# Kernel tuning notes

Hardware: AMD Instinct MI355X
Metric: run time of the kernel (lower is better)

The kernel has to match this reference:

```python
import jax, jax.numpy as jnp
import numpy as np

B, L, H, HEADS = 32, 512, 1024, 16
LN_EPS = 1e-5
NEG_INF = -1e9


def _layernorm(x, g, b):
    m = jnp.mean(x, axis=-1, keepdims=True)
    v = jnp.mean(jnp.square(x - m), axis=-1, keepdims=True)
    return (x - m) * jax.lax.rsqrt(v + LN_EPS) * g + b


def setup_inputs() -> dict:
    key = jax.random.key(0)
    ks = jax.random.split(key, 10)
    # deterministic variable graph sizes -> padding mask with fixed total valid count
    lengths = L - (np.arange(B) % 16) * 8          # per-graph node counts
    mask_np = np.arange(L)[None, :] < lengths[:, None]   # [B, L] bool
    node_idx = np.nonzero(mask_np.reshape(-1))[0].astype(np.int32)  # [14464]
    s = 0.02
    inp = {
        "x_dense": jax.random.normal(ks[0], (B, L, H), jnp.float32),
        "batch_CLS": jax.random.normal(ks[1], (B, 1, H), jnp.float32),
        "mask": jnp.asarray(mask_np),
        "node_idx": jnp.asarray(node_idx),
        "WQ": jax.random.normal(ks[2], (H, H), jnp.float32) * s,
        "bQ": jnp.zeros((H,), jnp.float32),
        "WK": jax.random.normal(ks[3], (H, H), jnp.float32) * s,
        "bK": jnp.zeros((H,), jnp.float32),
        "WV": jax.random.normal(ks[4], (H, H), jnp.float32) * s,
        "bV": jnp.zeros((H,), jnp.float32),
        "WO": jax.random.normal(ks[5], (H, H), jnp.float32) * s,
        "bO": jnp.zeros((H,), jnp.float32),
        "g1": jnp.ones((H,), jnp.float32),
        "beta1": jnp.zeros((H,), jnp.float32),
        "Wf1": jax.random.normal(ks[6], (H, 2 * H), jnp.float32) * s,
        "bf1": jnp.zeros((2 * H,), jnp.float32),
        "Wf2": jax.random.normal(ks[7], (2 * H, H), jnp.float32) * s,
        "bf2": jnp.zeros((H,), jnp.float32),
        "g2": jnp.ones((H,), jnp.float32),
        "beta2": jnp.zeros((H,), jnp.float32),
    }
    return inp


def reference(x_dense, batch_CLS, mask, node_idx, WQ, bQ, WK, bK, WV, bV,
              WO, bO, g1, beta1, Wf1, bf1, Wf2, bf2, g2, beta2):
    b, l, h = x_dense.shape
    d = h // HEADS
    # append CLS token; attention mask gets an always-True CLS column
    xd = jnp.concatenate([x_dense, batch_CLS], axis=1)            # [B, S, H], S = L+1
    am = jnp.concatenate([mask, jnp.ones((b, 1), bool)], axis=1)  # [B, S]
    S = l + 1
    Qh = (xd @ WQ + bQ).reshape(b, S, HEADS, d)
    Kh = (xd @ WK + bK).reshape(b, S, HEADS, d)
    Vh = (xd @ WV + bV).reshape(b, S, HEADS, d)
    scores = jnp.einsum('bqhd,bkhd->bhqk', Qh, Kh) / jnp.sqrt(jnp.float32(d))
    # additive padding mask over keys (masked_attention=True, clustering=False)
    scores = scores + jnp.where(am, 0.0, NEG_INF)[:, None, None, :]
    A = jax.nn.softmax(scores, axis=-1)                           # [B, h, S, S]
    # torch layout: A_torch[hh*B + b] == A[b, hh] -> cls_attn [h*B, S]
    cls_attn = jax.lax.stop_gradient(
        jnp.transpose(A[:, :, -1, :], (1, 0, 2)).reshape(HEADS * b, S))
    ctx = jnp.einsum('bhqk,bkhd->bqhd', A, Vh).reshape(b, S, h)
    attn_out = ctx @ WO + bO + xd                                  # residual
    cls_rows = attn_out[:, -1, :]                                  # [B, H]
    nodes = attn_out[:, :-1, :].reshape(b * l, h)[node_idx]        # valid nodes packed
    packed = jnp.concatenate([nodes, cls_rows], axis=0)            # [Ntot+B, H]
    h1 = _layernorm(packed, g1, beta1)
    ffn = jax.nn.relu(h1 @ Wf1 + bf1) @ Wf2 + bf2
    out = _layernorm(ffn + h1, g2, beta2)
    return out, cls_attn
```

## Files before the change

### kernel.cpp

```cpp
#include <hip/hip_runtime.h>
#include <stdint.h>

typedef unsigned short ushort_t;
typedef __bf16 bf16x8 __attribute__((ext_vector_type(8)));
typedef float  f32x4  __attribute__((ext_vector_type(4)));
typedef unsigned short ushortx8 __attribute__((ext_vector_type(8)));

constexpr int CB  = 32;
constexpr int CL  = 512;
constexpr int CNH = 16;
constexpr int CDH = 64;
constexpr int CS  = 513;
constexpr int CNR = CB * CS;
constexpr int CVTS = 576;
constexpr int CST = 136;

__device__ __forceinline__ float bf2f(ushort_t u) {
  return __builtin_bit_cast(float, (uint32_t)u << 16);
}
__device__ __forceinline__ ushort_t f2bf(float f) {
  __bf16 h = (__bf16)f;
  return __builtin_bit_cast(ushort_t, h);
}

typedef __attribute__((address_space(1))) const unsigned int GU32;
typedef __attribute__((address_space(3))) unsigned int LU32;
__device__ __forceinline__ void gld16(const void* g, void* l) {
  __builtin_amdgcn_global_load_lds((GU32*)g, (LU32*)l, 16, 0, 0);
}

__global__ __launch_bounds__(256)
void k_prep(const float* __restrict__ WQ, const float* __restrict__ WK,
            const float* __restrict__ WV, const float* __restrict__ WO,
            const float* __restrict__ Wf1, const float* __restrict__ Wf2,
            ushort_t* __restrict__ Wqkvt, ushort_t* __restrict__ Wot,
            ushort_t* __restrict__ Wf1t, ushort_t* __restrict__ Wf2t,
            const float* __restrict__ bQ, const float* __restrict__ bK,
            const float* __restrict__ bV, float* __restrict__ bqkv,
            int* __restrict__ lens, int* __restrict__ starts,
            const int* __restrict__ node_idx, int nn,
            const float* __restrict__ xd, const float* __restrict__ cls,
            ushort_t* __restrict__ XDP) {
  const int bid = blockIdx.x;
  const int t = threadIdx.x;
  if (bid == 8192) {
    for (int i = t; i < 3072; i += 256)
      bqkv[i] = (i < 1024) ? bQ[i] : (i < 2048 ? bK[i - 1024] : bV[i - 2048]);
    if (t < CB) {
      int bounds[2];
#pragma unroll
      for (int e = 0; e < 2; ++e) {
        int target = (t + e) << 9;
        int lo = 0, hi = nn;
        while (lo < hi) {
          int mid = (lo + hi) >> 1;
          if (node_idx[mid] < target) lo = mid + 1; else hi = mid;
        }
        bounds[e] = lo;
      }
      starts[t] = bounds[0];
      lens[t] = bounds[1] - bounds[0];
    }
    return;
  }
  if (bid > 8192) {
    size_t e = ((size_t)(bid - 8193) * 256 + t) * 8;
    int p = (int)(e >> 10);
    int col = (int)(e & 1023);
    const float* src = (p < nn) ? (xd + ((size_t)node_idx[p] << 10) + col)
                                : (cls + ((size_t)(p - nn) << 10) + col);
    float4 v0 = ((const float4*)src)[0];
    float4 v1 = ((const float4*)src)[1];
    ushortx8 o;
    o[0] = f2bf(v0.x); o[1] = f2bf(v0.y); o[2] = f2bf(v0.z); o[3] = f2bf(v0.w);
    o[4] = f2bf(v1.x); o[5] = f2bf(v1.y); o[6] = f2bf(v1.z); o[7] = f2bf(v1.w);
    *((ushortx8*)(XDP + e)) = o;
    return;
  }
  const float* in; ushort_t* out; int R, C, tx32, ty32;
  if (bid < 3072) {
    int which = bid >> 10, tt = bid & 1023;
    in = (which == 0) ? WQ : (which == 1 ? WK : WV);
    out = Wqkvt + (size_t)which * 1024 * 1024;
    R = 1024; C = 1024; tx32 = tt & 31; ty32 = tt >> 5;
  } else if (bid < 4096) {
    int tt = bid - 3072;
    in = WO; out = Wot; R = 1024; C = 1024; tx32 = tt & 31; ty32 = tt >> 5;
  } else if (bid < 6144) {
    int tt = bid - 4096;
    in = Wf1; out = Wf1t; R = 1024; C = 2048; tx32 = tt & 63; ty32 = tt >> 6;
  } else {
    int tt = bid - 6144;
    in = Wf2; out = Wf2t; R = 2048; C = 1024; tx32 = tt & 31; ty32 = tt >> 5;
  }
  __shared__ float tle[32][33];
  const int c0 = tx32 * 32, r0 = ty32 * 32;
  const int tx = t & 31, ty = t >> 5;
#pragma unroll
  for (int i = 0; i < 4; ++i) {
    int r = ty + i * 8;
    tle[r][tx] = in[(size_t)(r0 + r) * C + c0 + tx];
  }
  __syncthreads();
#pragma unroll
  for (int i = 0; i < 4; ++i) {
    int r = ty + i * 8;
    out[(size_t)(c0 + r) * R + r0 + tx] = f2bf(tle[tx][r]);
  }
}

template <int EPI>
__global__ __launch_bounds__(256, 2)
void k_gemm(const ushort_t* __restrict__ A, const ushort_t* __restrict__ Bt,
            int M, int N, int K,
            const float* __restrict__ pb,
            const ushort_t* __restrict__ pauxB,
            const int* __restrict__ nidx, int nn,
            ushort_t* __restrict__ outB0, ushort_t* __restrict__ outB1) {
  __shared__ __align__(16) ushort_t sh[128 * CST];
  ushort_t* As = sh;
  ushort_t* Bs = sh + 8192;
  const int tid = threadIdx.x;
  const int lane = tid & 63, wid = tid >> 6;
  const int wr = wid >> 1, wc = wid & 1;
  const int lm = lane & 15, lq = lane >> 4;
  const int m0 = blockIdx.y * 128, n0 = blockIdx.x * 128;

  f32x4 acc[4][4];
  const f32x4 z4 = {0.f, 0.f, 0.f, 0.f};
#pragma unroll
  for (int i = 0; i < 4; ++i)
#pragma unroll
    for (int j = 0; j < 4; ++j) acc[i][j] = z4;

  for (int kt = 0; kt < K; kt += 64) {
    __syncthreads();
#pragma unroll
    for (int it = 0; it < 4; ++it) {
      int c = it * 256 + tid;
      int r = c >> 3, jc = c & 7;
      int j = jc ^ (r & 7);
      int ra = m0 + r; if (ra > M - 1) ra = M - 1;
      gld16(A + (size_t)ra * K + kt + j * 8, As + (size_t)c * 8);
    }
#pragma unroll
    for (int it = 0; it < 4; ++it) {
      int c = it * 256 + tid;
      int r = c >> 3, jc = c & 7;
      int j = jc ^ (r & 7);
      gld16(Bt + (size_t)(n0 + r) * K + kt + j * 8, Bs + (size_t)c * 8);
    }
    __syncthreads();
#pragma unroll
    for (int kk = 0; kk < 2; ++kk) {
      bf16x8 af[4], bfr[4];
#pragma unroll
      for (int mi = 0; mi < 4; ++mi) {
        int R = wr * 64 + mi * 16 + lm;
        int u = R * 8 + ((kk * 4 + lq) ^ (R & 7));
        af[mi] = *reinterpret_cast<const bf16x8*>(As + u * 8);
      }
#pragma unroll
      for (int ni = 0; ni < 4; ++ni) {
        int R = wc * 64 + ni * 16 + lm;
        int u = R * 8 + ((kk * 4 + lq) ^ (R & 7));
        bfr[ni] = *reinterpret_cast<const bf16x8*>(Bs + u * 8);
      }
#pragma unroll
      for (int mi = 0; mi < 4; ++mi)
#pragma unroll
        for (int ni = 0; ni < 4; ++ni)
          acc[mi][ni] = __builtin_amdgcn_mfma_f32_16x16x32_bf16(af[mi], bfr[ni], acc[mi][ni], 0, 0, 0);
    }
  }

  __syncthreads();
  ushort_t* Cs = sh;
#pragma unroll
  for (int mi = 0; mi < 4; ++mi) {
#pragma unroll
    for (int ni = 0; ni < 4; ++ni) {
#pragma unroll
      for (int j = 0; j < 4; ++j) {
        int row = wr * 64 + mi * 16 + lq * 4 + j;
        int c128 = wc * 64 + ni * 16 + lm;
        int r = m0 + row;
        int rc = r < M ? r : M - 1;
        int c = n0 + c128;
        float v = acc[mi][ni][j] + pb[c];
        if constexpr (EPI == 1) v += bf2f(pauxB[(size_t)rc * 1024 + c]);
        else if constexpr (EPI == 2) v = v > 0.f ? v : 0.f;
        Cs[row * CST + c128] = f2bf(v);
      }
    }
  }
  __syncthreads();

  if (EPI == 0 && n0 >= 2048) {
    const int row = tid & 127;
    const int half = tid >> 7;
    const int r = m0 + row;
    if (r < M) {
      int b, s;
      if (r < nn) { int idx = nidx[r]; b = idx >> 9; s = idx & 511; }
      else        { b = r - nn; s = 512; }
      const int cvbase = n0 - 2048;
#pragma unroll 8
      for (int ci = 0; ci < 64; ++ci) {
        int c128 = half * 64 + ci;
        int cv = cvbase + c128;
        int h = cv >> 6, d = cv & 63;
        outB1[((size_t)(b * CNH + h) * CDH + d) * CVTS + s] = Cs[row * CST + c128];
      }
    }
  } else {
    const int ld = (EPI == 1) ? 1024 : 2048;
#pragma unroll
    for (int it = 0; it < 8; ++it) {
      int g = it * 256 + tid;
      int row = g >> 4, c16 = g & 15;
      int r = m0 + row;
      if (r >= M) continue;
      ushortx8 val = *reinterpret_cast<const ushortx8*>(&Cs[row * CST + c16 * 8]);
      *reinterpret_cast<ushortx8*>(&outB0[(size_t)r * ld + n0 + c16 * 8]) = val;
    }
  }
}

__global__ __launch_bounds__(256, 2)
void k_attn(const ushort_t* __restrict__ QK, const ushort_t* __restrict__ Vt,
            const int* __restrict__ lens, const int* __restrict__ starts, int nn,
            ushort_t* __restrict__ CTX) {
  __shared__ __align__(16) ushort_t Ks[64 * 64];
  __shared__ __align__(16) ushort_t Vs[64 * 64];
  __shared__ __align__(16) ushort_t Ps[4][16][72];

  const int tid = threadIdx.x;
  const int lane = tid & 63, wid = tid >> 6;
  const int lm = lane & 15, lq = lane >> 4;

  const int bidx = blockIdx.x;
  const int qt = bidx >> 9;
  const int hb = bidx & 511;
  const int h = hb & 15, b = hb >> 4;
  const int len = lens[b];
  if (qt * 128 >= len) return;
  const int st0 = starts[b];
  const int clsrow = nn + b;

  const int qbase = qt * 128 + wid * 16;

  bf16x8 aq[2][2];
#pragma unroll
  for (int t2 = 0; t2 < 2; ++t2) {
    int qr = qbase + t2 * 64 + lm; if (qr > len - 1) qr = len - 1;
    const ushort_t* qptr = QK + (size_t)(st0 + qr) * 2048 + h * CDH + lq * 8;
    aq[t2][0] = *reinterpret_cast<const bf16x8*>(qptr);
    aq[t2][1] = *reinterpret_cast<const bf16x8*>(qptr + 32);
  }

  const f32x4 z4 = {0.f, 0.f, 0.f, 0.f};
  f32x4 acc[2][4];
#pragma unroll
  for (int t2 = 0; t2 < 2; ++t2)
#pragma unroll
    for (int i = 0; i < 4; ++i) acc[t2][i] = z4;
  float lrow[2][4];
#pragma unroll
  for (int t2 = 0; t2 < 2; ++t2)
#pragma unroll
    for (int r2 = 0; r2 < 4; ++r2) lrow[t2][r2] = 0.f;

  const size_t vtBase = (size_t)(b * CNH + h) * CDH * CVTS;
  const float C1 = 0.125f * 1.44269504f;

  for (int kc = 0; kc < 9; ++kc) {
    const int k0 = kc * 64;
    if (k0 >= len && kc != 8) continue;
    const bool full = (k0 + 64 <= len);
    __syncthreads();
#pragma unroll
    for (int it = 0; it < 2; ++it) {
      int c = it * 256 + tid;
      int r = c >> 3, jc = c & 7;
      int j = jc ^ (r & 7);
      int k = k0 + r;
      int krow = (k < len) ? (st0 + k) : clsrow;
      gld16(QK + (size_t)krow * 2048 + 1024 + h * CDH + j * 8, Ks + (size_t)c * 8);
    }
#pragma unroll
    for (int it = 0; it < 2; ++it) {
      int c = it * 256 + tid;
      int r = c >> 3, jc = c & 7;
      int j = jc ^ (r & 7);
      gld16(Vt + vtBase + (size_t)r * CVTS + k0 + j * 8, Vs + (size_t)c * 8);
    }
    __syncthreads();

#pragma unroll
    for (int t2 = 0; t2 < 2; ++t2) {
      f32x4 sc[4];
#pragma unroll
      for (int st = 0; st < 4; ++st) sc[st] = z4;
#pragma unroll
      for (int kk = 0; kk < 2; ++kk) {
        bf16x8 kb[4];
#pragma unroll
        for (int st = 0; st < 4; ++st) {
          int R = st * 16 + lm;
          int u = R * 8 + ((kk * 4 + lq) ^ (R & 7));
          kb[st] = *reinterpret_cast<const bf16x8*>(Ks + u * 8);
        }
#pragma unroll
        for (int st = 0; st < 4; ++st)
          sc[st] = __builtin_amdgcn_mfma_f32_16x16x32_bf16(aq[t2][kk], kb[st], sc[st], 0, 0, 0);
      }

      if (full) {
#pragma unroll
        for (int st = 0; st < 4; ++st) {
#pragma unroll
          for (int r2 = 0; r2 < 4; ++r2) {
            float e = exp2f(sc[st][r2] * C1);
            lrow[t2][r2] += e;
            Ps[wid][lq * 4 + r2][st * 16 + lm] = f2bf(e);
          }
        }
      } else {
#pragma unroll
        for (int st = 0; st < 4; ++st) {
          int kg = k0 + st * 16 + lm;
          float madd = ((kg < len) || (kg == 512)) ? 0.f : -1e9f;
#pragma unroll
          for (int r2 = 0; r2 < 4; ++r2) {
            float e = exp2f(__builtin_fmaf(sc[st][r2], C1, madd));
            lrow[t2][r2] += e;
            Ps[wid][lq * 4 + r2][st * 16 + lm] = f2bf(e);
          }
        }
      }

      bf16x8 ap[2];
      ap[0] = *reinterpret_cast<const bf16x8*>(&Ps[wid][lm][lq * 8]);
      ap[1] = *reinterpret_cast<const bf16x8*>(&Ps[wid][lm][32 + lq * 8]);
#pragma unroll
      for (int kk = 0; kk < 2; ++kk) {
#pragma unroll
        for (int dt = 0; dt < 4; ++dt) {
          int R = dt * 16 + lm;
          int u = R * 8 + ((kk * 4 + lq) ^ (R & 7));
          bf16x8 vb = *reinterpret_cast<const bf16x8*>(Vs + u * 8);
          acc[t2][dt] = __builtin_amdgcn_mfma_f32_16x16x32_bf16(ap[kk], vb, acc[t2][dt], 0, 0, 0);
        }
      }
    }
  }

#pragma unroll
  for (int t2 = 0; t2 < 2; ++t2) {
    float inv[4];
#pragma unroll
    for (int r2 = 0; r2 < 4; ++r2) {
      float s0 = lrow[t2][r2];
      s0 += __shfl_xor(s0, 1);
      s0 += __shfl_xor(s0, 2);
      s0 += __shfl_xor(s0, 4);
      s0 += __shfl_xor(s0, 8);
      inv[r2] = 1.f / s0;
    }
#pragma unroll
    for (int dt = 0; dt < 4; ++dt) {
#pragma unroll
      for (int r2 = 0; r2 < 4; ++r2) {
        int q = qbase + t2 * 64 + lq * 4 + r2;
        if (q < len)
          CTX[(size_t)(st0 + q) * 1024 + h * CDH + dt * 16 + lm] = f2bf(acc[t2][dt][r2] * inv[r2]);
      }
    }
  }
}

__global__ __launch_bounds__(64)
void k_attn_cls(const ushort_t* __restrict__ QK, const ushort_t* __restrict__ Vt,
                const int* __restrict__ lens, const int* __restrict__ starts, int nn,
                ushort_t* __restrict__ CTX, float* __restrict__ clsOut) {
  const int bid = blockIdx.x;
  const int h = bid >> 5, b = bid & 31;
  const int l = threadIdx.x;
  __shared__ float qv[64];
  __shared__ float probs[516];
  const int st0 = starts[b];
  const int clsrow = nn + b;
  qv[l] = bf2f(QK[(size_t)clsrow * 2048 + h * CDH + l]);
  __syncthreads();
  const int len = lens[b];

  float sc[9];
  float mx = -INFINITY;
#pragma unroll
  for (int i = 0; i < 9; ++i) {
    int k = l + 64 * i;
    if (k < CS) {
      int krow = (k < len) ? (st0 + k) : clsrow;
      const ushort_t* kr = QK + (size_t)krow * 2048 + 1024 + h * CDH;
      float a2 = 0.f;
#pragma unroll
      for (int d0 = 0; d0 < 64; d0 += 8) {
        bf16x8 kv = *reinterpret_cast<const bf16x8*>(kr + d0);
#pragma unroll
        for (int j = 0; j < 8; ++j) a2 += qv[d0 + j] * (float)kv[j];
      }
      a2 *= 0.125f;
      if (!((k < len) || (k == 512))) a2 += -1e9f;
      sc[i] = a2;
      mx = fmaxf(mx, a2);
    } else {
      sc[i] = -INFINITY;
    }
  }
  for (int m2 = 1; m2 < 64; m2 <<= 1) mx = fmaxf(mx, __shfl_xor(mx, m2));
  float sum = 0.f, p[9];
#pragma unroll
  for (int i = 0; i < 9; ++i) { p[i] = __expf(sc[i] - mx); sum += p[i]; }
  for (int m2 = 1; m2 < 64; m2 <<= 1) sum += __shfl_xor(sum, m2);
  float invs = 1.f / sum;
#pragma unroll
  for (int i = 0; i < 9; ++i) {
    int k = l + 64 * i;
    if (k < CS) {
      float pr = p[i] * invs;
      clsOut[(size_t)bid * CS + k] = pr;
      probs[k] = pr;
    }
  }
  __syncthreads();
  const ushort_t* vr = Vt + ((size_t)(b * CNH + h) * CDH + l) * CVTS;
  float a2 = 0.f;
  for (int k = 0; k < 512; k += 8) {
    bf16x8 vv = *reinterpret_cast<const bf16x8*>(vr + k);
#pragma unroll
    for (int j = 0; j < 8; ++j) a2 += probs[k + j] * (float)vv[j];
  }
  a2 += probs[512] * bf2f(vr[512]);
  CTX[(size_t)clsrow * 1024 + h * CDH + l] = f2bf(a2);
}

template <int MODE>
__global__ __launch_bounds__(256)
void k_ln(const ushort_t* __restrict__ X,
          const float* __restrict__ g, const float* __restrict__ be,
          float* __restrict__ outF, ushort_t* __restrict__ outB) {
  const int p = blockIdx.x;
  const int t = threadIdx.x;
  const uint2 u = ((const uint2*)(X + (size_t)p * 1024))[t];
  float v0 = bf2f((ushort_t)(u.x & 0xffff)), v1 = bf2f((ushort_t)(u.x >> 16));
  float v2 = bf2f((ushort_t)(u.y & 0xffff)), v3 = bf2f((ushort_t)(u.y >> 16));
  float s1 = v0 + v1 + v2 + v3;
  float s2 = v0 * v0 + v1 * v1 + v2 * v2 + v3 * v3;
  for (int m2 = 1; m2 < 64; m2 <<= 1) {
    s1 += __shfl_xor(s1, m2);
    s2 += __shfl_xor(s2, m2);
  }
  __shared__ float red[8];
  const int lane = t & 63, wid = t >> 6;
  if (lane == 0) { red[wid] = s1; red[4 + wid] = s2; }
  __syncthreads();
  s1 = red[0] + red[1] + red[2] + red[3];
  s2 = red[4] + red[5] + red[6] + red[7];
  float mean = s1 * (1.f / 1024.f);
  float var = s2 * (1.f / 1024.f) - mean * mean;
  float rs = rsqrtf(var + 1e-5f);
  float4 gv = ((const float4*)g)[t];
  float4 bv = ((const float4*)be)[t];
  float y0 = (v0 - mean) * rs * gv.x + bv.x;
  float y1 = (v1 - mean) * rs * gv.y + bv.y;
  float y2 = (v2 - mean) * rs * gv.z + bv.z;
  float y3 = (v3 - mean) * rs * gv.w + bv.w;
  if constexpr (MODE == 0) {
    uint2 o;
    o.x = (unsigned)f2bf(y0) | ((unsigned)f2bf(y1) << 16);
    o.y = (unsigned)f2bf(y2) | ((unsigned)f2bf(y3) << 16);
    ((uint2*)(outB + (size_t)p * 1024))[t] = o;
  } else {
    ((float4*)(outF + (size_t)p * 1024))[t] = make_float4(y0, y1, y2, y3);
  }
}

extern "C" void kernel_launch(void* const* d_in, const int* in_sizes, int n_in,
                              void* d_out, int out_size, void* d_ws, size_t ws_size,
                              hipStream_t stream) {
  const float* x_dense = (const float*)d_in[0];
  const float* bcls    = (const float*)d_in[1];
  const int*   node_idx = (const int*)d_in[3];
  const float* WQ = (const float*)d_in[4];
  const float* bQ = (const float*)d_in[5];
  const float* WK = (const float*)d_in[6];
  const float* bK = (const float*)d_in[7];
  const float* WV = (const float*)d_in[8];
  const float* bV = (const float*)d_in[9];
  const float* WO = (const float*)d_in[10];
  const float* bO = (const float*)d_in[11];
  const float* g1 = (const float*)d_in[12];
  const float* be1 = (const float*)d_in[13];
  const float* Wf1 = (const float*)d_in[14];
  const float* bf1 = (const float*)d_in[15];
  const float* Wf2 = (const float*)d_in[16];
  const float* bf2 = (const float*)d_in[17];
  const float* g2 = (const float*)d_in[18];
  const float* be2 = (const float*)d_in[19];

  const int nn = in_sizes[3];
  const int NP = nn + CB;

  char* ws = (char*)d_ws;
  const size_t oWqkv = 0;
  const size_t oWo   = oWqkv + (size_t)3072 * 1024 * 2;
  const size_t oWf1  = oWo + (size_t)1024 * 1024 * 2;
  const size_t oWf2  = oWf1 + (size_t)2048 * 1024 * 2;
  const size_t oBqkv = oWf2 + (size_t)1024 * 2048 * 2;
  const size_t oLens = oBqkv + 3072 * 4;
  const size_t oRA = (oLens + 512 + 255) & ~(size_t)255;
  const size_t szRA = (size_t)CNR * 2048 * 2;
  const size_t oRB = oRA + szRA;
  const size_t szRB = (size_t)CNR * 1024 * 2;
  const size_t oRC = oRB + szRB;
  const size_t szVt = (size_t)CB * CNH * CDH * CVTS * 2;
  const size_t oRD = oRC + szVt;

  ushort_t* Wqkvt = (ushort_t*)(ws + oWqkv);
  ushort_t* Wot   = (ushort_t*)(ws + oWo);
  ushort_t* Wf1t  = (ushort_t*)(ws + oWf1);
  ushort_t* Wf2t  = (ushort_t*)(ws + oWf2);
  float* bqkv = (float*)(ws + oBqkv);
  int* lens   = (int*)(ws + oLens);
  int* starts = lens + CB;
  ushort_t* QK  = (ushort_t*)(ws + oRA);
  ushort_t* CTX = (ushort_t*)(ws + oRB);
  ushort_t* Vt  = (ushort_t*)(ws + oRC);
  ushort_t* XDP = (ushort_t*)(ws + oRD);
  ushort_t* AO  = (ushort_t*)(ws + oRA);
  ushort_t* H1B = (ushort_t*)(ws + oRB);
  ushort_t* G   = (ushort_t*)(ws + oRA);
  ushort_t* F   = (ushort_t*)(ws + oRC);

  float* out0 = (float*)d_out;
  float* clsOut = out0 + (size_t)NP * 1024;

  dim3 blk(256);
  hipMemsetAsync(Vt, 0, szVt, stream);

  const int nPack = NP / 2;
  k_prep<<<dim3(8193 + nPack), blk, 0, stream>>>(
      WQ, WK, WV, WO, Wf1, Wf2, Wqkvt, Wot, Wf1t, Wf2t,
      bQ, bK, bV, bqkv, lens, starts, node_idx, nn, x_dense, bcls, XDP);

  const int mtP = (NP + 127) / 128;
  k_gemm<0><<<dim3(3072 / 128, mtP), blk, 0, stream>>>(
      XDP, Wqkvt, NP, 3072, 1024, bqkv, nullptr, node_idx, nn, QK, Vt);
  k_attn<<<dim3(CB * CNH * 4), blk, 0, stream>>>(QK, Vt, lens, starts, nn, CTX);
  k_attn_cls<<<dim3(CB * CNH), dim3(64), 0, stream>>>(QK, Vt, lens, starts, nn, CTX, clsOut);
  k_gemm<1><<<dim3(1024 / 128, mtP), blk, 0, stream>>>(
      CTX, Wot, NP, 1024, 1024, bO, XDP, nullptr, nn, AO, nullptr);
  k_ln<0><<<dim3(NP), blk, 0, stream>>>(AO, g1, be1, nullptr, H1B);
  k_gemm<2><<<dim3(2048 / 128, mtP), blk, 0, stream>>>(
      H1B, Wf1t, NP, 2048, 1024, bf1, nullptr, nullptr, nn, G, nullptr);
  k_gemm<1><<<dim3(1024 / 128, mtP), blk, 0, stream>>>(
      G, Wf2t, NP, 1024, 2048, bf2, H1B, nullptr, nn, F, nullptr);
  k_ln<1><<<dim3(NP), blk, 0, stream>>>(F, g2, be2, out0, nullptr);
  (void)ws_size; (void)out_size; (void)n_in;
}
```

Measured before the change: 450.0 us.

## Store CLS value column next to valid keys and fold Vt zeroing into prep

The CLS token's V column now goes right after each graph's valid keys (slot len) instead of slot 512. This lets the attention kernel loop over only ceil((len+1)/64) key chunks rather than always visiting the last chunk. The separate hipMemsetAsync of Vt is replaced by extra zeroing blocks inside the prep kernel, which removes one launch. Masking is changed to kg <= len to match the new layout.

```diff
diff --git a/kernel.cpp b/kernel.cpp
--- a/kernel.cpp
+++ b/kernel.cpp
@@ -14,6 +14,7 @@
 constexpr int CNR = CB * CS;
 constexpr int CVTS = 576;
 constexpr int CST = 136;
+constexpr int CVTN = CB * CNH * CDH * CVTS;
 
 __device__ __forceinline__ float bf2f(ushort_t u) {
   return __builtin_bit_cast(float, (uint32_t)u << 16);
@@ -40,7 +41,7 @@
             int* __restrict__ lens, int* __restrict__ starts,
             const int* __restrict__ node_idx, int nn,
             const float* __restrict__ xd, const float* __restrict__ cls,
-            ushort_t* __restrict__ XDP) {
+            ushort_t* __restrict__ XDP, ushort_t* __restrict__ Vt, int nPack) {
   const int bid = blockIdx.x;
   const int t = threadIdx.x;
   if (bid == 8192) {
@@ -64,17 +65,28 @@
     return;
   }
   if (bid > 8192) {
-    size_t e = ((size_t)(bid - 8193) * 256 + t) * 8;
-    int p = (int)(e >> 10);
-    int col = (int)(e & 1023);
-    const float* src = (p < nn) ? (xd + ((size_t)node_idx[p] << 10) + col)
-                                : (cls + ((size_t)(p - nn) << 10) + col);
-    float4 v0 = ((const float4*)src)[0];
-    float4 v1 = ((const float4*)src)[1];
-    ushortx8 o;
-    o[0] = f2bf(v0.x); o[1] = f2bf(v0.y); o[2] = f2bf(v0.z); o[3] = f2bf(v0.w);
-    o[4] = f2bf(v1.x); o[5] = f2bf(v1.y); o[6] = f2bf(v1.z); o[7] = f2bf(v1.w);
-    *((ushortx8*)(XDP + e)) = o;
+    int pb2 = bid - 8193;
+    if (pb2 < nPack) {
+      size_t e = ((size_t)pb2 * 256 + t) * 8;
+      int p = (int)(e >> 10);
+      int col = (int)(e & 1023);
+      const float* src = (p < nn) ? (xd + ((size_t)node_idx[p] << 10) + col)
+                                  : (cls + ((size_t)(p - nn) << 10) + col);
+      float4 v0 = ((const float4*)src)[0];
+      float4 v1 = ((const float4*)src)[1];
+      ushortx8 o;
+      o[0] = f2bf(v0.x); o[1] = f2bf(v0.y); o[2] = f2bf(v0.z); o[3] = f2bf(v0.w);
+      o[4] = f2bf(v1.x); o[5] = f2bf(v1.y); o[6] = f2bf(v1.z); o[7] = f2bf(v1.w);
+      *((ushortx8*)(XDP + e)) = o;
+    } else {
+      int zb = pb2 - nPack;
+      const ushortx8 z = {0, 0, 0, 0, 0, 0, 0, 0};
+#pragma unroll
+      for (int i = 0; i < 4; ++i) {
+        size_t off = (size_t)zb * 8192 + i * 2048 + t * 8;
+        if (off < (size_t)CVTN) *((ushortx8*)(Vt + off)) = z;
+      }
+    }
     return;
   }
   const float* in; ushort_t* out; int R, C, tx32, ty32;
@@ -115,7 +127,7 @@
             int M, int N, int K,
             const float* __restrict__ pb,
             const ushort_t* __restrict__ pauxB,
-            const int* __restrict__ nidx, int nn,
+            const int* __restrict__ nidx, const int* __restrict__ plens, int nn,
             ushort_t* __restrict__ outB0, ushort_t* __restrict__ outB1) {
   __shared__ __align__(16) ushort_t sh[128 * CST];
   ushort_t* As = sh;
@@ -203,7 +215,7 @@
     if (r < M) {
       int b, s;
       if (r < nn) { int idx = nidx[r]; b = idx >> 9; s = idx & 511; }
-      else        { b = r - nn; s = 512; }
+      else        { b = r - nn; s = plens[b]; }
       const int cvbase = n0 - 2048;
 #pragma unroll 8
       for (int ci = 0; ci < 64; ++ci) {
@@ -273,10 +285,10 @@
 
   const size_t vtBase = (size_t)(b * CNH + h) * CDH * CVTS;
   const float C1 = 0.125f * 1.44269504f;
-
-  for (int kc = 0; kc < 9; ++kc) {
+  const int NC = (len + 64) >> 6;
+
+  for (int kc = 0; kc < NC; ++kc) {
     const int k0 = kc * 64;
-    if (k0 >= len && kc != 8) continue;
     const bool full = (k0 + 64 <= len);
     __syncthreads();
 #pragma unroll
@@ -330,7 +342,7 @@
 #pragma unroll
         for (int st = 0; st < 4; ++st) {
           int kg = k0 + st * 16 + lm;
-          float madd = ((kg < len) || (kg == 512)) ? 0.f : -1e9f;
+          float madd = (kg <= len) ? 0.f : -1e9f;
 #pragma unroll
           for (int r2 = 0; r2 < 4; ++r2) {
             float e = exp2f(__builtin_fmaf(sc[st][r2], C1, madd));
@@ -441,7 +453,7 @@
 #pragma unroll
     for (int j = 0; j < 8; ++j) a2 += probs[k + j] * (float)vv[j];
   }
-  a2 += probs[512] * bf2f(vr[512]);
+  a2 += probs[512] * bf2f(vr[len]);
   CTX[(size_t)clsrow * 1024 + h * CDH + l] = f2bf(a2);
 }
 
@@ -524,7 +536,7 @@
   const size_t oRB = oRA + szRA;
   const size_t szRB = (size_t)CNR * 1024 * 2;
   const size_t oRC = oRB + szRB;
-  const size_t szVt = (size_t)CB * CNH * CDH * CVTS * 2;
+  const size_t szVt = (size_t)CVTN * 2;
   const size_t oRD = oRC + szVt;
 
   ushort_t* Wqkvt = (ushort_t*)(ws + oWqkv);
@@ -547,25 +559,24 @@
   float* clsOut = out0 + (size_t)NP * 1024;
 
   dim3 blk(256);
-  hipMemsetAsync(Vt, 0, szVt, stream);
-
   const int nPack = NP / 2;
-  k_prep<<<dim3(8193 + nPack), blk, 0, stream>>>(
+  const int nZero = (CVTN + 8191) / 8192;
+  k_prep<<<dim3(8193 + nPack + nZero), blk, 0, stream>>>(
       WQ, WK, WV, WO, Wf1, Wf2, Wqkvt, Wot, Wf1t, Wf2t,
-      bQ, bK, bV, bqkv, lens, starts, node_idx, nn, x_dense, bcls, XDP);
+      bQ, bK, bV, bqkv, lens, starts, node_idx, nn, x_dense, bcls, XDP, Vt, nPack);
 
   const int mtP = (NP + 127) / 128;
   k_gemm<0><<<dim3(3072 / 128, mtP), blk, 0, stream>>>(
-      XDP, Wqkvt, NP, 3072, 1024, bqkv, nullptr, node_idx, nn, QK, Vt);
+      XDP, Wqkvt, NP, 3072, 1024, bqkv, nullptr, node_idx, lens, nn, QK, Vt);
   k_attn<<<dim3(CB * CNH * 4), blk, 0, stream>>>(QK, Vt, lens, starts, nn, CTX);
   k_attn_cls<<<dim3(CB * CNH), dim3(64), 0, stream>>>(QK, Vt, lens, starts, nn, CTX, clsOut);
   k_gemm<1><<<dim3(1024 / 128, mtP), blk, 0, stream>>>(
-      CTX, Wot, NP, 1024, 1024, bO, XDP, nullptr, nn, AO, nullptr);
+      CTX, Wot, NP, 1024, 1024, bO, XDP, nullptr, nullptr, nn, AO, nullptr);
   k_ln<0><<<dim3(NP), blk, 0, stream>>>(AO, g1, be1, nullptr, H1B);
   k_gemm<2><<<dim3(2048 / 128, mtP), blk, 0, stream>>>(
-      H1B, Wf1t, NP, 2048, 1024, bf1, nullptr, nullptr, nn, G, nullptr);
+      H1B, Wf1t, NP, 2048, 1024, bf1, nullptr, nullptr, nullptr, nn, G, nullptr);
   k_gemm<1><<<dim3(1024 / 128, mtP), blk, 0, stream>>>(
-      G, Wf2t, NP, 1024, 2048, bf2, H1B, nullptr, nn, F, nullptr);
+      G, Wf2t, NP, 1024, 2048, bf2, H1B, nullptr, nullptr, nn, F, nullptr);
   k_ln<1><<<dim3(NP), blk, 0, stream>>>(F, g2, be2, out0, nullptr);
   (void)ws_size; (void)out_size; (void)n_in;
 }
```

Measured after the change: 437.8 us. 1.03x faster.
